# Kernel optimization log

Hardware: AMD Instinct MI355X
Metric: run time of the kernel (lower is better)

The kernel has to match this reference:

```python
import jax, jax.numpy as jnp
import numpy as np

B, N_TOTAL = 4096, 512
DIMS = {"RT": (8, 8, 16), "OB": (8, 8, 16), "RS": (8, 8, 16), "TG": (16, 16, 32)}


def _branch(obs, W, b, dq, dk):
    # obs: [B, n, 2]; fused QKV projection then self-attention + mean pool
    P = obs @ W + b                              # [B, n, dq+dk+dv]
    Q, K, V = P[..., :dq], P[..., dq:dq + dk], P[..., dq + dk:]
    scores = jnp.einsum('bqd,bkd->bqk', Q, K) / (dk ** 0.5)
    A = jax.nn.softmax(scores, axis=-1)
    return jnp.mean(jnp.einsum('bqk,bkv->bqv', A, V), axis=1)  # [B, dv]


def setup_inputs() -> dict:
    key = jax.random.key(0)
    ks = jax.random.split(key, 16)
    inp = {"state": jax.random.normal(ks[0], (B, N_TOTAL, 3), jnp.float32),
           "num_rt": 128, "num_ob": 128, "num_rs": 128, "num_tg": 128}
    i = 1
    for name, (dq, dk, dv) in DIMS.items():
        inp[f"W_{name}"] = 0.1 * jax.random.normal(ks[i], (2, dq + dk + dv), jnp.float32)
        inp[f"b_{name}"] = jnp.zeros((dq + dk + dv,), jnp.float32)
        i += 1
    dcat = sum(d[2] for d in DIMS.values())  # 64
    inp["W1"] = 0.1 * jax.random.normal(ks[i], (dcat, 256), jnp.float32)
    inp["b1"] = jnp.zeros((256,), jnp.float32)
    inp["W2"] = 0.1 * jax.random.normal(ks[i + 1], (256, 256), jnp.float32)
    inp["b2"] = jnp.zeros((256,), jnp.float32)
    inp["W3"] = 0.01 * jax.random.normal(ks[i + 2], (256, 1), jnp.float32)
    inp["b3"] = jnp.zeros((1,), jnp.float32)
    return inp


def reference(state, num_rt, num_ob, num_rs, num_tg,
              W_RT, b_RT, W_OB, b_OB, W_RS, b_RS, W_TG, b_TG,
              W1, b1, W2, b2, W3, b3):
    o0, o1 = 0, num_rt
    o2, o3 = o1 + num_ob, o1 + num_ob + num_rs
    o4 = o3 + num_tg
    h_rt = _branch(state[:, o0:o1, 0:2], W_RT, b_RT, *DIMS["RT"][:2])
    h_ob = _branch(state[:, o1:o2, 0:2], W_OB, b_OB, *DIMS["OB"][:2])
    h_rs = _branch(state[:, o2:o3, 0:2], W_RS, b_RS, *DIMS["RS"][:2])
    h_tg = _branch(state[:, o3:o4, 0:2], W_TG, b_TG, *DIMS["TG"][:2])
    h = jnp.concatenate([h_rt, h_ob, h_rs, h_tg], axis=1)  # [B, 64]
    h = jnp.tanh(h @ W1 + b1)
    h = jnp.tanh(h @ W2 + b2)
    return h @ W3 + b3  # [B, 1]
```

## Files before the change

kernel.cpp:

```cpp
#include <hip/hip_runtime.h>

#define LOG2E 1.44269504088896340736f

typedef float v2f __attribute__((ext_vector_type(2)));

__device__ __forceinline__ float fexp2(float x){
#if __has_builtin(__builtin_amdgcn_exp2f)
  return __builtin_amdgcn_exp2f(x);
#else
  return exp2f(x);
#endif
}
__device__ __forceinline__ float frcp(float x){
#if __has_builtin(__builtin_amdgcn_rcpf)
  return __builtin_amdgcn_rcpf(x);
#else
  return 1.0f/x;
#endif
}
__device__ __forceinline__ float tanh_fast(float x){
  float e = fexp2(x * (2.0f*LOG2E));
  return 1.0f - 2.0f*frcp(e + 1.0f);
}
__device__ __forceinline__ float4 fma4(float s, float4 w, float4 a){
  a.x = fmaf(s,w.x,a.x); a.y = fmaf(s,w.y,a.y);
  a.z = fmaf(s,w.z,a.z); a.w = fmaf(s,w.w,a.w);
  return a;
}
__device__ __forceinline__ v2f vfma2(v2f a, v2f b, v2f c){
#if __has_builtin(__builtin_elementwise_fma)
  return __builtin_elementwise_fma(a,b,c);
#else
  v2f r; r.x=fmaf(a.x,b.x,c.x); r.y=fmaf(a.y,b.y,c.y); return r;
#endif
}

template<int DQ, int DV, int NB>
__device__ __forceinline__ void branch_all(
    const float* __restrict__ state, int b0, int n0,
    const float* __restrict__ W, const float* __restrict__ bias,
    float* __restrict__ sA, float* __restrict__ sB, float* __restrict__ sYv,
    float* __restrict__ sHbase, int hoff, float* __restrict__ hbuf,
    int lane, int tix)
{
  const int D = 4*DQ;
  const float qs = LOG2E * (DQ==8 ? 0.35355339059327373f : 0.25f);

  float M00=0,M01=0,M02=0,M10=0,M11=0,M12=0,M20=0,M21=0,M22=0;
  #pragma unroll
  for (int d=0; d<DQ; ++d) {
    float aq0 = W[d], aq1 = W[D+d], aq2 = bias[d];
    float ak0 = W[DQ+d], ak1 = W[D+DQ+d], ak2 = bias[DQ+d];
    M00 = fmaf(aq0,ak0,M00); M01 = fmaf(aq0,ak1,M01); M02 = fmaf(aq0,ak2,M02);
    M10 = fmaf(aq1,ak0,M10); M11 = fmaf(aq1,ak1,M11); M12 = fmaf(aq1,ak2,M12);
    M20 = fmaf(aq2,ak0,M20); M21 = fmaf(aq2,ak1,M21); M22 = fmaf(aq2,ak2,M22);
  }
  M00*=qs; M01*=qs; M02*=qs; M10*=qs; M11*=qs; M12*=qs; M20*=qs; M21*=qs; M22*=qs;

  float wv0 = 0.f, wv1 = 0.f, vb = 0.f;
  if (lane < DV) { wv0 = W[2*DQ+lane]; wv1 = W[D+2*DQ+lane]; vb = bias[2*DQ+lane]; }

  #pragma unroll 1
  for (int e = 0; e < NB; ++e) {
    const int b = b0 + e;
    const float* sp = state + ((size_t)b*512 + (size_t)(n0 + lane))*3;
    float x0 = sp[0],   y0 = sp[1];
    float x1 = sp[192], y1 = sp[193];

    {
      int p = lane >> 1, h = lane & 1;
      float ux = fmaf(M00,x0, fmaf(M01,y0, M02));
      float uy = fmaf(M10,x0, fmaf(M11,y0, M12));
      float uz = fmaf(M20,x0, fmaf(M21,y0, M22));
      sA[p*4 + h]     = ux;  sA[p*4 + 2 + h] = uy;
      sB[p*4 + h]     = uz;  sB[p*4 + 2 + h] = x0;
      sYv[lane]       = y0;
      int p1 = p + 32;
      float vx = fmaf(M00,x1, fmaf(M01,y1, M02));
      float vy = fmaf(M10,x1, fmaf(M11,y1, M12));
      float vz = fmaf(M20,x1, fmaf(M21,y1, M22));
      sA[p1*4 + h]     = vx;  sA[p1*4 + 2 + h] = vy;
      sB[p1*4 + h]     = vz;  sB[p1*4 + 2 + h] = x1;
      sYv[lane + 64]   = y1;
    }
    __syncthreads();

    v2f X0; X0.x=x0; X0.y=x0;  v2f Y0; Y0.x=y0; Y0.y=y0;
    v2f X1; X1.x=x1; X1.y=x1;  v2f Y1; Y1.x=y1; Y1.y=y1;
    v2f E0={0.f,0.f}, Ex0={0.f,0.f}, Ey0={0.f,0.f};
    v2f E1={0.f,0.f}, Ex1={0.f,0.f}, Ey1={0.f,0.f};
    const float4* A4 = (const float4*)sA;
    const float4* B4 = (const float4*)sB;
    const float4* Y4 = (const float4*)sYv;
    #pragma unroll 2
    for (int pp = 0; pp < 32; ++pp) {
      float4 Av0 = A4[2*pp], Av1 = A4[2*pp+1];
      float4 Bv0 = B4[2*pp], Bv1 = B4[2*pp+1];
      float4 Yq  = Y4[pp];
      {
        v2f ux; ux.x=Av0.x; ux.y=Av0.y;  v2f uy; uy.x=Av0.z; uy.y=Av0.w;
        v2f uz; uz.x=Bv0.x; uz.y=Bv0.y;  v2f xk; xk.x=Bv0.z; xk.y=Bv0.w;
        v2f yk; yk.x=Yq.x;  yk.y=Yq.y;
        v2f s0 = vfma2(X0, ux, vfma2(Y0, uy, uz));
        v2f s1 = vfma2(X1, ux, vfma2(Y1, uy, uz));
        v2f e0, e1;
        e0.x = fexp2(s0.x); e0.y = fexp2(s0.y);
        e1.x = fexp2(s1.x); e1.y = fexp2(s1.y);
        E0 += e0; Ex0 = vfma2(e0, xk, Ex0); Ey0 = vfma2(e0, yk, Ey0);
        E1 += e1; Ex1 = vfma2(e1, xk, Ex1); Ey1 = vfma2(e1, yk, Ey1);
      }
      {
        v2f ux; ux.x=Av1.x; ux.y=Av1.y;  v2f uy; uy.x=Av1.z; uy.y=Av1.w;
        v2f uz; uz.x=Bv1.x; uz.y=Bv1.y;  v2f xk; xk.x=Bv1.z; xk.y=Bv1.w;
        v2f yk; yk.x=Yq.z;  yk.y=Yq.w;
        v2f s0 = vfma2(X0, ux, vfma2(Y0, uy, uz));
        v2f s1 = vfma2(X1, ux, vfma2(Y1, uy, uz));
        v2f e0, e1;
        e0.x = fexp2(s0.x); e0.y = fexp2(s0.y);
        e1.x = fexp2(s1.x); e1.y = fexp2(s1.y);
        E0 += e0; Ex0 = vfma2(e0, xk, Ex0); Ey0 = vfma2(e0, yk, Ey0);
        E1 += e1; Ex1 = vfma2(e1, xk, Ex1); Ey1 = vfma2(e1, yk, Ey1);
      }
    }
    float r0 = frcp(E0.x + E0.y), r1 = frcp(E1.x + E1.y);
    float gx = fmaf(Ex0.x + Ex0.y, r0, (Ex1.x + Ex1.y) * r1);
    float gy = fmaf(Ey0.x + Ey0.y, r0, (Ey1.x + Ey1.y) * r1);
    #pragma unroll
    for (int m=1; m<64; m<<=1) {
      gx += __shfl_xor(gx, m, 64);
      gy += __shfl_xor(gy, m, 64);
    }
    gx *= 0.0078125f;
    gy *= 0.0078125f;
    if (lane < DV) sHbase[hoff + lane] = fmaf(gx, wv0, fmaf(gy, wv1, vb));
    __syncthreads();
    if (tix < 80) hbuf[(size_t)b*80 + tix] = sHbase[tix];
  }
}

__global__ __launch_bounds__(256)
void attn_kernel(const float* __restrict__ state,
    const float* __restrict__ W_RT, const float* __restrict__ b_RT,
    const float* __restrict__ W_OB, const float* __restrict__ b_OB,
    const float* __restrict__ W_RS, const float* __restrict__ b_RS,
    const float* __restrict__ W_TG, const float* __restrict__ b_TG,
    float* __restrict__ hbuf)
{
  __shared__ float sA[4][256] __attribute__((aligned(16)));
  __shared__ float sB[4][256] __attribute__((aligned(16)));
  __shared__ float sY[4][128] __attribute__((aligned(16)));
  __shared__ float sH[80];
  const int b0   = blockIdx.x * 4;
  const int wave = threadIdx.x >> 6;
  const int lane = threadIdx.x & 63;

  const float* W;  const float* bb;
  if      (wave == 0) { W = W_RT; bb = b_RT; }
  else if (wave == 1) { W = W_OB; bb = b_OB; }
  else if (wave == 2) { W = W_RS; bb = b_RS; }
  else                { W = W_TG; bb = b_TG; }
  const int n0 = wave * 128;
  const int hoff = wave * 16;

  if (wave < 3)
    branch_all<8 ,16,4>(state, b0, n0, W, bb, sA[wave], sB[wave], sY[wave],
                        sH, hoff, hbuf, lane, threadIdx.x);
  else
    branch_all<16,32,4>(state, b0, n0, W, bb, sA[wave], sB[wave], sY[wave],
                        sH, hoff, hbuf, lane, threadIdx.x);
}

__global__ __launch_bounds__(256, 1)
void mlp_kernel(const float* __restrict__ hbuf,
    const float* __restrict__ W1, const float* __restrict__ b1,
    const float* __restrict__ W2, const float* __restrict__ b2,
    const float* __restrict__ W3, const float* __restrict__ b3,
    float* __restrict__ out)
{
  __shared__ float sHin[16][84];
  __shared__ float sH1[16][260];
  __shared__ float sRed[4][16];
  const int t  = threadIdx.x;
  const int b0 = blockIdx.x * 16;
  const int q  = t >> 2;
  const int rg = t & 3;
  const int wave = t >> 6;

  for (int i = t; i < 16*80; i += 256) sHin[i/80][i%80] = hbuf[(size_t)b0*80 + i];
  __syncthreads();

  const float4* W1v = (const float4*)W1;
  const float4* W2v = (const float4*)W2;

  float4 acc[4];
  {
    float4 bq = ((const float4*)b1)[q];
    acc[0]=bq; acc[1]=bq; acc[2]=bq; acc[3]=bq;
    float4 wb[4][4];
    #pragma unroll
    for (int p=0; p<4; ++p)
      #pragma unroll
      for (int jj=0; jj<4; ++jj) wb[p][jj] = W1v[(size_t)(4*p+jj)*64 + q];
    #pragma unroll 4
    for (int i4 = 0; i4 < 16; ++i4) {
      float4 w0=wb[i4&3][0], w1=wb[i4&3][1], w2=wb[i4&3][2], w3=wb[i4&3][3];
      #pragma unroll
      for (int jj=0; jj<4; ++jj) wb[i4&3][jj] = W1v[(size_t)((i4+4)*4+jj)*64 + q];
      #pragma unroll
      for (int r=0; r<4; ++r) {
        float4 h = *(const float4*)&sHin[4*rg+r][i4*4];
        acc[r] = fma4(h.x,w0, fma4(h.y,w1, fma4(h.z,w2, fma4(h.w,w3, acc[r]))));
      }
    }
    #pragma unroll
    for (int i4 = 16; i4 < 20; ++i4) {
      float4 w0=wb[i4&3][0], w1=wb[i4&3][1], w2=wb[i4&3][2], w3=wb[i4&3][3];
      #pragma unroll
      for (int r=0; r<4; ++r) {
        float4 h = *(const float4*)&sHin[4*rg+r][i4*4];
        acc[r] = fma4(h.x,w0, fma4(h.y,w1, fma4(h.z,w2, fma4(h.w,w3, acc[r]))));
      }
    }
  }
  #pragma unroll
  for (int r=0; r<4; ++r) {
    float4 o;
    o.x=tanh_fast(acc[r].x); o.y=tanh_fast(acc[r].y);
    o.z=tanh_fast(acc[r].z); o.w=tanh_fast(acc[r].w);
    *(float4*)&sH1[4*rg+r][4*q] = o;
  }
  __syncthreads();

  float4 acc2[4];
  {
    float4 bq = ((const float4*)b2)[q];
    acc2[0]=bq; acc2[1]=bq; acc2[2]=bq; acc2[3]=bq;
    float4 wb[4][4];
    #pragma unroll
    for (int p=0; p<4; ++p)
      #pragma unroll
      for (int jj=0; jj<4; ++jj) wb[p][jj] = W2v[(size_t)(4*p+jj)*64 + q];
    #pragma unroll 4
    for (int i4 = 0; i4 < 60; ++i4) {
      float4 w0=wb[i4&3][0], w1=wb[i4&3][1], w2=wb[i4&3][2], w3=wb[i4&3][3];
      #pragma unroll
      for (int jj=0; jj<4; ++jj) wb[i4&3][jj] = W2v[(size_t)((i4+4)*4+jj)*64 + q];
      #pragma unroll
      for (int r=0; r<4; ++r) {
        float4 h = *(const float4*)&sH1[4*rg+r][i4*4];
        acc2[r] = fma4(h.x,w0, fma4(h.y,w1, fma4(h.z,w2, fma4(h.w,w3, acc2[r]))));
      }
    }
    #pragma unroll
    for (int i4 = 60; i4 < 64; ++i4) {
      float4 w0=wb[i4&3][0], w1=wb[i4&3][1], w2=wb[i4&3][2], w3=wb[i4&3][3];
      #pragma unroll
      for (int r=0; r<4; ++r) {
        float4 h = *(const float4*)&sH1[4*rg+r][i4*4];
        acc2[r] = fma4(h.x,w0, fma4(h.y,w1, fma4(h.z,w2, fma4(h.w,w3, acc2[r]))));
      }
    }
  }

  float4 w3v = ((const float4*)W3)[q];
  float p[4];
  #pragma unroll
  for (int r=0; r<4; ++r) {
    p[r] = tanh_fast(acc2[r].x)*w3v.x + tanh_fast(acc2[r].y)*w3v.y
         + tanh_fast(acc2[r].z)*w3v.z + tanh_fast(acc2[r].w)*w3v.w;
  }
  #pragma unroll
  for (int m=4; m<64; m<<=1) {
    #pragma unroll
    for (int r=0; r<4; ++r) p[r] += __shfl_xor(p[r], m, 64);
  }
  if ((t & 63) == rg) {
    #pragma unroll
    for (int r=0; r<4; ++r) sRed[wave][4*rg + r] = p[r];
  }
  __syncthreads();
  if (t < 16)
    out[b0 + t] = sRed[0][t] + sRed[1][t] + sRed[2][t] + sRed[3][t] + b3[0];
}

extern "C" void kernel_launch(void* const* d_in, const int* in_sizes, int n_in,
                              void* d_out, int out_size, void* d_ws, size_t ws_size,
                              hipStream_t stream) {
  const float* state = (const float*)d_in[0];
  const float* W_RT = (const float*)d_in[5];
  const float* b_RT = (const float*)d_in[6];
  const float* W_OB = (const float*)d_in[7];
  const float* b_OB = (const float*)d_in[8];
  const float* W_RS = (const float*)d_in[9];
  const float* b_RS = (const float*)d_in[10];
  const float* W_TG = (const float*)d_in[11];
  const float* b_TG = (const float*)d_in[12];
  const float* W1 = (const float*)d_in[13];
  const float* b1 = (const float*)d_in[14];
  const float* W2 = (const float*)d_in[15];
  const float* b2 = (const float*)d_in[16];
  const float* W3 = (const float*)d_in[17];
  const float* b3 = (const float*)d_in[18];

  float* hbuf = (float*)d_ws;

  attn_kernel<<<1024, 256, 0, stream>>>(state,
      W_RT, b_RT, W_OB, b_OB, W_RS, b_RS, W_TG, b_TG, hbuf);
  mlp_kernel<<<256, 256, 0, stream>>>(hbuf, W1, b1, W2, b2, W3, b3,
      (float*)d_out);
}
```

Baseline: 65.14 us.

## Split attention kernel into single-wave blocks per branch, removing block barriers

The attention kernel now launches 8192 one-wave blocks. Each block handles one branch for two batch rows, replacing 256-thread blocks where four waves handled the four branches for four rows. Because each block is a single wave, the __syncthreads calls and the shared staging of h before the global store go away, and each wave writes its slice of hbuf directly. Shared data is repacked into one float4 (u.x, u.y, u.z, x) per key plus a separate y array. Packed v2f FMA math is replaced by scalar FMAs, and the branch dimensions become runtime values instead of template parameters, which may cost some ALU throughput in the exp-bound inner loop.

```diff
diff --git a/kernel.cpp b/kernel.cpp
--- a/kernel.cpp
+++ b/kernel.cpp
@@ -1,8 +1,6 @@
 #include <hip/hip_runtime.h>
 
 #define LOG2E 1.44269504088896340736f
-
-typedef float v2f __attribute__((ext_vector_type(2)));
 
 __device__ __forceinline__ float fexp2(float x){
 #if __has_builtin(__builtin_amdgcn_exp2f)
@@ -27,118 +25,8 @@
   a.z = fmaf(s,w.z,a.z); a.w = fmaf(s,w.w,a.w);
   return a;
 }
-__device__ __forceinline__ v2f vfma2(v2f a, v2f b, v2f c){
-#if __has_builtin(__builtin_elementwise_fma)
-  return __builtin_elementwise_fma(a,b,c);
-#else
-  v2f r; r.x=fmaf(a.x,b.x,c.x); r.y=fmaf(a.y,b.y,c.y); return r;
-#endif
-}
-
-template<int DQ, int DV, int NB>
-__device__ __forceinline__ void branch_all(
-    const float* __restrict__ state, int b0, int n0,
-    const float* __restrict__ W, const float* __restrict__ bias,
-    float* __restrict__ sA, float* __restrict__ sB, float* __restrict__ sYv,
-    float* __restrict__ sHbase, int hoff, float* __restrict__ hbuf,
-    int lane, int tix)
-{
-  const int D = 4*DQ;
-  const float qs = LOG2E * (DQ==8 ? 0.35355339059327373f : 0.25f);
-
-  float M00=0,M01=0,M02=0,M10=0,M11=0,M12=0,M20=0,M21=0,M22=0;
-  #pragma unroll
-  for (int d=0; d<DQ; ++d) {
-    float aq0 = W[d], aq1 = W[D+d], aq2 = bias[d];
-    float ak0 = W[DQ+d], ak1 = W[D+DQ+d], ak2 = bias[DQ+d];
-    M00 = fmaf(aq0,ak0,M00); M01 = fmaf(aq0,ak1,M01); M02 = fmaf(aq0,ak2,M02);
-    M10 = fmaf(aq1,ak0,M10); M11 = fmaf(aq1,ak1,M11); M12 = fmaf(aq1,ak2,M12);
-    M20 = fmaf(aq2,ak0,M20); M21 = fmaf(aq2,ak1,M21); M22 = fmaf(aq2,ak2,M22);
-  }
-  M00*=qs; M01*=qs; M02*=qs; M10*=qs; M11*=qs; M12*=qs; M20*=qs; M21*=qs; M22*=qs;
-
-  float wv0 = 0.f, wv1 = 0.f, vb = 0.f;
-  if (lane < DV) { wv0 = W[2*DQ+lane]; wv1 = W[D+2*DQ+lane]; vb = bias[2*DQ+lane]; }
-
-  #pragma unroll 1
-  for (int e = 0; e < NB; ++e) {
-    const int b = b0 + e;
-    const float* sp = state + ((size_t)b*512 + (size_t)(n0 + lane))*3;
-    float x0 = sp[0],   y0 = sp[1];
-    float x1 = sp[192], y1 = sp[193];
-
-    {
-      int p = lane >> 1, h = lane & 1;
-      float ux = fmaf(M00,x0, fmaf(M01,y0, M02));
-      float uy = fmaf(M10,x0, fmaf(M11,y0, M12));
-      float uz = fmaf(M20,x0, fmaf(M21,y0, M22));
-      sA[p*4 + h]     = ux;  sA[p*4 + 2 + h] = uy;
-      sB[p*4 + h]     = uz;  sB[p*4 + 2 + h] = x0;
-      sYv[lane]       = y0;
-      int p1 = p + 32;
-      float vx = fmaf(M00,x1, fmaf(M01,y1, M02));
-      float vy = fmaf(M10,x1, fmaf(M11,y1, M12));
-      float vz = fmaf(M20,x1, fmaf(M21,y1, M22));
-      sA[p1*4 + h]     = vx;  sA[p1*4 + 2 + h] = vy;
-      sB[p1*4 + h]     = vz;  sB[p1*4 + 2 + h] = x1;
-      sYv[lane + 64]   = y1;
-    }
-    __syncthreads();
-
-    v2f X0; X0.x=x0; X0.y=x0;  v2f Y0; Y0.x=y0; Y0.y=y0;
-    v2f X1; X1.x=x1; X1.y=x1;  v2f Y1; Y1.x=y1; Y1.y=y1;
-    v2f E0={0.f,0.f}, Ex0={0.f,0.f}, Ey0={0.f,0.f};
-    v2f E1={0.f,0.f}, Ex1={0.f,0.f}, Ey1={0.f,0.f};
-    const float4* A4 = (const float4*)sA;
-    const float4* B4 = (const float4*)sB;
-    const float4* Y4 = (const float4*)sYv;
-    #pragma unroll 2
-    for (int pp = 0; pp < 32; ++pp) {
-      float4 Av0 = A4[2*pp], Av1 = A4[2*pp+1];
-      float4 Bv0 = B4[2*pp], Bv1 = B4[2*pp+1];
-      float4 Yq  = Y4[pp];
-      {
-        v2f ux; ux.x=Av0.x; ux.y=Av0.y;  v2f uy; uy.x=Av0.z; uy.y=Av0.w;
-        v2f uz; uz.x=Bv0.x; uz.y=Bv0.y;  v2f xk; xk.x=Bv0.z; xk.y=Bv0.w;
-        v2f yk; yk.x=Yq.x;  yk.y=Yq.y;
-        v2f s0 = vfma2(X0, ux, vfma2(Y0, uy, uz));
-        v2f s1 = vfma2(X1, ux, vfma2(Y1, uy, uz));
-        v2f e0, e1;
-        e0.x = fexp2(s0.x); e0.y = fexp2(s0.y);
-        e1.x = fexp2(s1.x); e1.y = fexp2(s1.y);
-        E0 += e0; Ex0 = vfma2(e0, xk, Ex0); Ey0 = vfma2(e0, yk, Ey0);
-        E1 += e1; Ex1 = vfma2(e1, xk, Ex1); Ey1 = vfma2(e1, yk, Ey1);
-      }
-      {
-        v2f ux; ux.x=Av1.x; ux.y=Av1.y;  v2f uy; uy.x=Av1.z; uy.y=Av1.w;
-        v2f uz; uz.x=Bv1.x; uz.y=Bv1.y;  v2f xk; xk.x=Bv1.z; xk.y=Bv1.w;
-        v2f yk; yk.x=Yq.z;  yk.y=Yq.w;
-        v2f s0 = vfma2(X0, ux, vfma2(Y0, uy, uz));
-        v2f s1 = vfma2(X1, ux, vfma2(Y1, uy, uz));
-        v2f e0, e1;
-        e0.x = fexp2(s0.x); e0.y = fexp2(s0.y);
-        e1.x = fexp2(s1.x); e1.y = fexp2(s1.y);
-        E0 += e0; Ex0 = vfma2(e0, xk, Ex0); Ey0 = vfma2(e0, yk, Ey0);
-        E1 += e1; Ex1 = vfma2(e1, xk, Ex1); Ey1 = vfma2(e1, yk, Ey1);
-      }
-    }
-    float r0 = frcp(E0.x + E0.y), r1 = frcp(E1.x + E1.y);
-    float gx = fmaf(Ex0.x + Ex0.y, r0, (Ex1.x + Ex1.y) * r1);
-    float gy = fmaf(Ey0.x + Ey0.y, r0, (Ey1.x + Ey1.y) * r1);
-    #pragma unroll
-    for (int m=1; m<64; m<<=1) {
-      gx += __shfl_xor(gx, m, 64);
-      gy += __shfl_xor(gy, m, 64);
-    }
-    gx *= 0.0078125f;
-    gy *= 0.0078125f;
-    if (lane < DV) sHbase[hoff + lane] = fmaf(gx, wv0, fmaf(gy, wv1, vb));
-    __syncthreads();
-    if (tix < 80) hbuf[(size_t)b*80 + tix] = sHbase[tix];
-  }
-}
-
-__global__ __launch_bounds__(256)
+
+__global__ __launch_bounds__(64, 8)
 void attn_kernel(const float* __restrict__ state,
     const float* __restrict__ W_RT, const float* __restrict__ b_RT,
     const float* __restrict__ W_OB, const float* __restrict__ b_OB,
@@ -146,28 +34,88 @@
     const float* __restrict__ W_TG, const float* __restrict__ b_TG,
     float* __restrict__ hbuf)
 {
-  __shared__ float sA[4][256] __attribute__((aligned(16)));
-  __shared__ float sB[4][256] __attribute__((aligned(16)));
-  __shared__ float sY[4][128] __attribute__((aligned(16)));
-  __shared__ float sH[80];
-  const int b0   = blockIdx.x * 4;
-  const int wave = threadIdx.x >> 6;
-  const int lane = threadIdx.x & 63;
-
-  const float* W;  const float* bb;
-  if      (wave == 0) { W = W_RT; bb = b_RT; }
-  else if (wave == 1) { W = W_OB; bb = b_OB; }
-  else if (wave == 2) { W = W_RS; bb = b_RS; }
-  else                { W = W_TG; bb = b_TG; }
-  const int n0 = wave * 128;
-  const int hoff = wave * 16;
-
-  if (wave < 3)
-    branch_all<8 ,16,4>(state, b0, n0, W, bb, sA[wave], sB[wave], sY[wave],
-                        sH, hoff, hbuf, lane, threadIdx.x);
-  else
-    branch_all<16,32,4>(state, b0, n0, W, bb, sA[wave], sB[wave], sY[wave],
-                        sH, hoff, hbuf, lane, threadIdx.x);
+  __shared__ float4 su4[128];
+  __shared__ float  sy[128] __attribute__((aligned(16)));
+  const int bid  = blockIdx.x;
+  const int br   = bid & 3;
+  const int b0   = (bid >> 2) * 2;
+  const int lane = threadIdx.x;
+
+  const float* W;  const float* bb;  int dq;
+  if      (br == 0) { W = W_RT; bb = b_RT; dq = 8;  }
+  else if (br == 1) { W = W_OB; bb = b_OB; dq = 8;  }
+  else if (br == 2) { W = W_RS; bb = b_RS; dq = 8;  }
+  else              { W = W_TG; bb = b_TG; dq = 16; }
+  const int D  = 4*dq;
+  const int dv = 2*dq;
+  const int n0 = br * 128;
+  const int hoff = br * 16;
+  const float qs = LOG2E * (dq==8 ? 0.35355339059327373f : 0.25f);
+
+  float M00=0,M01=0,M02=0,M10=0,M11=0,M12=0,M20=0,M21=0,M22=0;
+  for (int d=0; d<dq; ++d) {
+    float aq0 = W[d], aq1 = W[D+d], aq2 = bb[d];
+    float ak0 = W[dq+d], ak1 = W[D+dq+d], ak2 = bb[dq+d];
+    M00 = fmaf(aq0,ak0,M00); M01 = fmaf(aq0,ak1,M01); M02 = fmaf(aq0,ak2,M02);
+    M10 = fmaf(aq1,ak0,M10); M11 = fmaf(aq1,ak1,M11); M12 = fmaf(aq1,ak2,M12);
+    M20 = fmaf(aq2,ak0,M20); M21 = fmaf(aq2,ak1,M21); M22 = fmaf(aq2,ak2,M22);
+  }
+  M00*=qs; M01*=qs; M02*=qs; M10*=qs; M11*=qs; M12*=qs; M20*=qs; M21*=qs; M22*=qs;
+
+  float wv0 = 0.f, wv1 = 0.f, vb = 0.f;
+  if (lane < dv) { wv0 = W[2*dq+lane]; wv1 = W[D+2*dq+lane]; vb = bb[2*dq+lane]; }
+
+  #pragma unroll 1
+  for (int e = 0; e < 2; ++e) {
+    const int b = b0 + e;
+    const float* sp = state + ((size_t)b*512 + (size_t)(n0 + lane))*3;
+    float x0 = sp[0],   y0 = sp[1];
+    float x1 = sp[192], y1 = sp[193];
+
+    {
+      float4 uA, uB;
+      uA.x = fmaf(M00,x0, fmaf(M01,y0, M02));
+      uA.y = fmaf(M10,x0, fmaf(M11,y0, M12));
+      uA.z = fmaf(M20,x0, fmaf(M21,y0, M22));
+      uA.w = x0;
+      uB.x = fmaf(M00,x1, fmaf(M01,y1, M02));
+      uB.y = fmaf(M10,x1, fmaf(M11,y1, M12));
+      uB.z = fmaf(M20,x1, fmaf(M21,y1, M22));
+      uB.w = x1;
+      su4[lane]    = uA;  sy[lane]    = y0;
+      su4[lane+64] = uB;  sy[lane+64] = y1;
+    }
+
+    float E0=0.f, Ex0=0.f, Ey0=0.f, E1=0.f, Ex1=0.f, Ey1=0.f;
+    const float4* Y4 = (const float4*)sy;
+    #pragma unroll 2
+    for (int k4=0; k4<32; ++k4) {
+      float4 yq = Y4[k4];
+      #pragma unroll
+      for (int j=0; j<4; ++j) {
+        float4 u = su4[4*k4+j];
+        float yk = (j==0)?yq.x : (j==1)?yq.y : (j==2)?yq.z : yq.w;
+        float s0 = fmaf(x0,u.x, fmaf(y0,u.y, u.z));
+        float s1 = fmaf(x1,u.x, fmaf(y1,u.y, u.z));
+        float e0 = fexp2(s0), e1 = fexp2(s1);
+        E0 += e0;                 E1 += e1;
+        Ex0 = fmaf(e0,u.w,Ex0);   Ex1 = fmaf(e1,u.w,Ex1);
+        Ey0 = fmaf(e0,yk,Ey0);    Ey1 = fmaf(e1,yk,Ey1);
+      }
+    }
+    float r0 = frcp(E0), r1 = frcp(E1);
+    float gx = fmaf(Ex0,r0, Ex1*r1);
+    float gy = fmaf(Ey0,r0, Ey1*r1);
+    #pragma unroll
+    for (int m=1; m<64; m<<=1) {
+      gx += __shfl_xor(gx, m, 64);
+      gy += __shfl_xor(gy, m, 64);
+    }
+    gx *= 0.0078125f;
+    gy *= 0.0078125f;
+    if (lane < dv)
+      hbuf[(size_t)b*80 + hoff + lane] = fmaf(gx, wv0, fmaf(gy, wv1, vb));
+  }
 }
 
 __global__ __launch_bounds__(256, 1)
@@ -304,7 +252,7 @@
 
   float* hbuf = (float*)d_ws;
 
-  attn_kernel<<<1024, 256, 0, stream>>>(state,
+  attn_kernel<<<8192, 64, 0, stream>>>(state,
       W_RT, b_RT, W_OB, b_OB, W_RS, b_RS, W_TG, b_TG, hbuf);
   mlp_kernel<<<256, 256, 0, stream>>>(hbuf, W1, b1, W2, b2, W3, b3,
       (float*)d_out);
```

After: 76.55 us. 17.5% more time.
